# Kernel optimization log

Hardware: AMD Instinct MI355X
Metric: run time of the kernel (lower is better)

The kernel has to match this reference:

```python
import jax, jax.numpy as jnp
import numpy as np

D_MODEL, D_FF, N_EXPERTS, TOP_K = 512, 2048, 8, 2


def setup_inputs() -> dict:
    key = jax.random.key(0)
    ks = jax.random.split(key, 7)
    B, S = 2, 2048
    x = jax.random.normal(ks[0], (B, S, D_MODEL), dtype=jnp.float32)
    s1 = 1.0 / np.sqrt(D_MODEL)
    s2 = 1.0 / np.sqrt(D_FF)
    Wg = jax.random.normal(ks[1], (D_MODEL, N_EXPERTS), dtype=jnp.float32) * s1
    bg = jnp.zeros((N_EXPERTS,), dtype=jnp.float32)
    W1 = jax.random.normal(ks[2], (N_EXPERTS, D_MODEL, D_FF), dtype=jnp.float32) * s1
    b1 = jax.random.normal(ks[3], (N_EXPERTS, D_FF), dtype=jnp.float32) * s1
    W2 = jax.random.normal(ks[4], (N_EXPERTS, D_FF, D_MODEL), dtype=jnp.float32) * s2
    b2 = jax.random.normal(ks[5], (N_EXPERTS, D_MODEL), dtype=jnp.float32) * s2
    return {"x": x, "Wg": Wg, "bg": bg, "W1": W1, "b1": b1, "W2": W2, "b2": b2}


def reference(x, Wg, bg, W1, b1, W2, b2):
    B, S, D = x.shape
    xt = x.reshape(B * S, D)  # [T, D]
    # gating
    gate_logits = xt @ Wg + bg                      # [T, E]
    gate_scores = jax.nn.softmax(gate_logits, axis=-1)
    topk_scores, topk_idx = jax.lax.top_k(gate_scores, TOP_K)  # [T, K]
    topk_scores = topk_scores / jnp.sum(topk_scores, axis=-1, keepdims=True)
    # combine weights per expert: [T, E]
    combine = jnp.sum(jax.nn.one_hot(topk_idx, N_EXPERTS, dtype=xt.dtype)
                      * topk_scores[..., None], axis=1)
    # dense per-expert MLP (exact GELU, dropout is identity in eval)
    h = jax.nn.gelu(jnp.einsum('td,edf->etf', xt, W1) + b1[:, None, :],
                    approximate=False)             # [E, T, F]
    expert_out = jnp.einsum('etf,efd->etd', h, W2) + b2[:, None, :]  # [E, T, D]
    out = jnp.einsum('te,etd->td', combine, expert_out)
    return out.reshape(B, S, D)
```

## Files before the change

### kernel.cpp

```cpp
#include <hip/hip_runtime.h>
#include <hip/hip_bf16.h>
#include <math.h>

#define D_MODEL 512
#define D_FF    2048
#define NEXP    8
#define NXCD    8

using bf16x8 = __attribute__((ext_vector_type(8))) short;
using f32x4  = __attribute__((ext_vector_type(4))) float;

__device__ inline unsigned short f2bf(float x) {
    __hip_bfloat16 h = __float2bfloat16(x);
    unsigned short u; __builtin_memcpy(&u, &h, 2); return u;
}
__device__ inline unsigned pk(float a, float b) {
    return (unsigned)f2bf(a) | ((unsigned)f2bf(b) << 16);
}
__device__ inline float erf_fast(float x) {
    float ax = fabsf(x);
    float t  = 1.f / fmaf(0.3275911f, ax, 1.f);
    float p  = t * fmaf(t, fmaf(t, fmaf(t, fmaf(t, 1.061405429f, -1.453152027f),
                                        1.421413741f), -0.284496736f), 0.254829592f);
    float r  = 1.f - p * __expf(-ax * ax);
    return copysignf(r, x);
}
__device__ inline float gelu_exact(float v) {
    return 0.5f * v * (1.f + erf_fast(v * 0.70710678118654752f));
}
__device__ inline void gload_lds16(const void* g, void* l) {
    __builtin_amdgcn_global_load_lds(
        (const __attribute__((address_space(1))) unsigned int*)g,
        (__attribute__((address_space(3))) unsigned int*)l, 16, 0, 0);
}

__global__ __launch_bounds__(256) void gate_kernel(
    const float* __restrict__ x, const float* __restrict__ Wg,
    const float* __restrict__ bg,
    int2* __restrict__ tk_e, float2* __restrict__ tk_s,
    unsigned short* __restrict__ Xb, int T)
{
    int lane = threadIdx.x & 63;
    int w    = threadIdx.x >> 6;
    int t    = blockIdx.x * 4 + w;
    if (t >= T) return;

    const float* xr = x + (size_t)t * D_MODEL;
    unsigned short* xbr = Xb ? (Xb + (size_t)t * D_MODEL) : nullptr;
    float lg[NEXP];
#pragma unroll
    for (int e = 0; e < NEXP; e++) lg[e] = 0.f;

#pragma unroll
    for (int it = 0; it < D_MODEL / 64; it++) {
        int d = lane + 64 * it;
        float xv = xr[d];
        if (xbr) xbr[d] = f2bf(xv);
        const float* wr = Wg + (size_t)d * NEXP;
#pragma unroll
        for (int e = 0; e < NEXP; e++) lg[e] += xv * wr[e];
    }
#pragma unroll
    for (int off = 32; off > 0; off >>= 1) {
#pragma unroll
        for (int e = 0; e < NEXP; e++) lg[e] += __shfl_xor(lg[e], off, 64);
    }

    if (lane == 0) {
#pragma unroll
        for (int e = 0; e < NEXP; e++) lg[e] += bg[e];
        int e0 = 0;
#pragma unroll
        for (int e = 1; e < NEXP; e++) if (lg[e] > lg[e0]) e0 = e;
        int e1 = (e0 == 0) ? 1 : 0;
#pragma unroll
        for (int e = 0; e < NEXP; e++) if (e != e0 && lg[e] > lg[e1]) e1 = e;
        float s0 = 1.f / (1.f + expf(lg[e1] - lg[e0]));
        tk_e[t] = make_int2(e0, e1);
        tk_s[t] = make_float2(s0, 1.f - s0);
    }
}

__global__ __launch_bounds__(256) void route_kernel(
    const int2* __restrict__ tk_e, const float2* __restrict__ tk_s,
    int* __restrict__ counts, int* __restrict__ ltok, float* __restrict__ lsc,
    int2* __restrict__ tk_pos, int T)
{
    int t    = blockIdx.x * 256 + threadIdx.x;
    int lane = threadIdx.x & 63;
    bool valid = t < T;
    int2   es = valid ? tk_e[t] : make_int2(-1, -1);
    float2 ss = valid ? tk_s[t] : make_float2(0.f, 0.f);
    int ppos[2] = {0, 0};

#pragma unroll
    for (int slot = 0; slot < 2; slot++) {
        int   e = slot ? es.y : es.x;
        float s = slot ? ss.y : ss.x;
#pragma unroll
        for (int ex = 0; ex < NEXP; ex++) {
            unsigned long long m = __ballot(e == ex);
            if (m == 0ull) continue;
            int leader = __ffsll((long long)m) - 1;
            int base = 0;
            if (lane == leader) base = atomicAdd(&counts[ex], __popcll(m));
            base = __shfl(base, leader, 64);
            if (e == ex) {
                int pos = base + __popcll(m & ((1ull << lane) - 1ull));
                ltok[(size_t)ex * T + pos] = t;
                lsc [(size_t)ex * T + pos] = s;
                ppos[slot] = pos | (ex << 16);
            }
        }
    }
    if (valid) tk_pos[t] = make_int2(ppos[0], ppos[1]);
}

__global__ void prefix_kernel(const int* __restrict__ counts, int* __restrict__ offs)
{
    if (threadIdx.x == 0) {
        int acc = 0;
        for (int e = 0; e < NEXP; e++) { offs[e] = acc; acc += counts[e]; }
        offs[NEXP] = acc;
    }
}

__global__ __launch_bounds__(256) void tcvt2_kernel(
    const float* __restrict__ W1, const float* __restrict__ W2,
    unsigned short* __restrict__ W1t, unsigned short* __restrict__ W2t)
{
    __shared__ unsigned short tile[64][72];
    int z = blockIdx.y;
    bool isw2 = z >= NEXP;
    int e = z & (NEXP - 1);
    int R = isw2 ? D_FF : D_MODEL;
    int C = isw2 ? D_MODEL : D_FF;
    const float* src = isw2 ? W2 : W1;
    unsigned short* dst = isw2 ? W2t : W1t;

    int nx  = C / 64;
    int lin = blockIdx.x;
    int r0 = (lin / nx) * 64, c0 = (lin % nx) * 64;

    const float* s = src + ((size_t)e * R + r0) * C + c0;
    unsigned short* d = dst + ((size_t)e * C + c0) * R + r0;
    int t = threadIdx.x;
#pragma unroll
    for (int i = 0; i < 4; i++) {
        int idx = t + 256 * i;
        int r = idx >> 4, c4 = (idx & 15) * 4;
        float4 v = *(const float4*)(s + (size_t)r * C + c4);
        tile[c4    ][r] = f2bf(v.x);
        tile[c4 + 1][r] = f2bf(v.y);
        tile[c4 + 2][r] = f2bf(v.z);
        tile[c4 + 3][r] = f2bf(v.w);
    }
    __syncthreads();
#pragma unroll
    for (int i = 0; i < 2; i++) {
        int idx = t + 256 * i;
        int c = idx >> 3, q = idx & 7;
        uint4 v = *(const uint4*)(&tile[c][q * 8]);
        *(uint4*)(d + (size_t)c * R + q * 8) = v;
    }
}

__global__ __launch_bounds__(256, 4) void moe_gemm1(
    const unsigned short* __restrict__ Xb,
    const unsigned short* __restrict__ W1t, const float* __restrict__ b1,
    const int* __restrict__ counts, const int* __restrict__ offs,
    const int* __restrict__ ltok,
    unsigned short* __restrict__ Hg, int T)
{
    int nwg  = gridDim.x;
    int bid  = blockIdx.x;
    int work = (bid % NXCD) * (nwg / NXCD) + bid / NXCD;
    int perexp = nwg / NEXP;
    int e    = work / perexp;
    int rem  = work % perexp;
    int mbase = (rem >> 4) * 128;
    int fb    = (rem & 15) * 128;

    int n = counts[e];
    if (mbase >= n) return;
    int off = offs[e];

    __shared__ __align__(16) unsigned char SB[2][16384];
    __shared__ int toks_s[128];

    int tid = threadIdx.x, lane = tid & 63, w = tid >> 6;
    int wr = w & 1, wc = w >> 1;

    if (tid < 128) {
        int idx = mbase + tid; if (idx > n - 1) idx = n - 1;
        toks_s[tid] = ltok[(size_t)e * T + idx];
    }
    __syncthreads();

    const unsigned short* W1te = W1t + (size_t)e * D_FF * D_MODEL;
    int c = lane & 7, rsub = lane >> 3;

    const char* aptr[4]; const char* bptr[4]; int soff[4];
#pragma unroll
    for (int j = 0; j < 4; j++) {
        int r  = j * 32 + w * 8 + rsub;
        int sc = c ^ (r & 7);
        aptr[j] = (const char*)(Xb + (size_t)toks_s[r] * D_MODEL) + sc * 16;
        bptr[j] = (const char*)(W1te + (size_t)(fb + r) * D_MODEL) + sc * 16;
        soff[j] = (j * 32 + w * 8) * 128;
    }

    f32x4 acc[4][4];
#pragma unroll
    for (int i = 0; i < 4; i++)
#pragma unroll
        for (int j = 0; j < 4; j++) acc[i][j] = (f32x4){0.f, 0.f, 0.f, 0.f};

    for (int kc = 0; kc < D_MODEL; kc += 64) {
#pragma unroll
        for (int j = 0; j < 4; j++) gload_lds16(aptr[j] + kc * 2, SB[0] + soff[j]);
#pragma unroll
        for (int j = 0; j < 4; j++) gload_lds16(bptr[j] + kc * 2, SB[1] + soff[j]);
        __syncthreads();

#pragma unroll
        for (int ks = 0; ks < 2; ks++) {
            bf16x8 av[4], bv[4];
            int kbyte = ks * 64 + ((lane >> 4) * 16);
#pragma unroll
            for (int i = 0; i < 4; i++) {
                int row = wr * 64 + i * 16 + (lane & 15);
                av[i] = *(const bf16x8*)(SB[0] + row * 128 + (kbyte ^ ((row & 7) << 4)));
            }
#pragma unroll
            for (int j = 0; j < 4; j++) {
                int fr = wc * 64 + j * 16 + (lane & 15);
                bv[j] = *(const bf16x8*)(SB[1] + fr * 128 + (kbyte ^ ((fr & 7) << 4)));
            }
#pragma unroll
            for (int i = 0; i < 4; i++)
#pragma unroll
                for (int j = 0; j < 4; j++)
                    acc[i][j] = __builtin_amdgcn_mfma_f32_16x16x32_bf16(av[i], bv[j], acc[i][j], 0, 0, 0);
        }
        __syncthreads();
    }

    char* Eb = (char*)&SB[0][0];
    const float* b1e = b1 + (size_t)e * D_FF;
#pragma unroll
    for (int j = 0; j < 4; j++) {
        int col = wc * 64 + j * 16 + (lane & 15);
        float b1v = b1e[fb + col];
#pragma unroll
        for (int i = 0; i < 4; i++) {
#pragma unroll
            for (int r = 0; r < 4; r++) {
                int row = wr * 64 + i * 16 + (lane >> 4) * 4 + r;
                float v = gelu_exact(acc[i][j][r] + b1v);
                *(unsigned short*)(Eb + row * 256 + ((col * 2) ^ ((row & 7) << 4))) = f2bf(v);
            }
        }
    }
    __syncthreads();
#pragma unroll
    for (int k = 0; k < 8; k++) {
        int idx = tid + 256 * k;
        int row = idx >> 4, ch = idx & 15;
        if (mbase + row < n) {
            uint4 v = *(const uint4*)(Eb + row * 256 + ((ch * 16) ^ ((row & 7) << 4)));
            *(uint4*)(Hg + (size_t)(off + mbase + row) * D_FF + fb + ch * 8) = v;
        }
    }
}

__global__ __launch_bounds__(256, 4) void moe_gemm2_og(
    const unsigned short* __restrict__ Hg,
    const unsigned short* __restrict__ W2t, const float* __restrict__ b2,
    const int* __restrict__ counts, const int* __restrict__ offs,
    const int* __restrict__ ltok, const float* __restrict__ lsc,
    float* __restrict__ Og, int T)
{
    int nwg  = gridDim.x;
    int bid  = blockIdx.x;
    int work = (bid % NXCD) * (nwg / NXCD) + bid / NXCD;
    int perexp = nwg / NEXP;
    int e    = work / perexp;
    int rem  = work % perexp;
    int mbase = (rem >> 3) * 128;
    int z    = rem & 7;
    int nb   = z & 3, kb = z >> 2;
    int db   = nb * 128;

    int n = counts[e];
    if (mbase >= n) return;
    int off = offs[e];

    __shared__ __align__(16) unsigned char HsB[128 * 128];
    __shared__ __align__(16) unsigned char WsB[128 * 128];
    __shared__ float scs_s[128];

    int tid = threadIdx.x, lane = tid & 63, w = tid >> 6;
    int wr = w & 1, wc = w >> 1;

    if (tid < 128) {
        int idx = mbase + tid; if (idx > n - 1) idx = n - 1;
        scs_s[tid] = lsc[(size_t)e * T + idx];
    }
    __syncthreads();

    const unsigned short* W2te = W2t + (size_t)e * D_MODEL * D_FF;
    int c = lane & 7, rsub = lane >> 3;

    const char* aptr[4]; const char* bptr[4]; int soff[4];
#pragma unroll
    for (int j = 0; j < 4; j++) {
        int r = j * 32 + w * 8 + rsub;
        int srow = mbase + r; if (srow > n - 1) srow = n - 1;
        int sc = c ^ (r & 7);
        aptr[j] = (const char*)(Hg + (size_t)(off + srow) * D_FF) + sc * 16;
        bptr[j] = (const char*)(W2te + (size_t)(db + r) * D_FF) + sc * 16;
        soff[j] = (j * 32 + w * 8) * 128;
    }

    f32x4 acc[4][4];
#pragma unroll
    for (int i = 0; i < 4; i++)
#pragma unroll
        for (int j = 0; j < 4; j++) acc[i][j] = (f32x4){0.f, 0.f, 0.f, 0.f};

    int kbase = kb * 1024;
    for (int kc = 0; kc < 1024; kc += 64) {
        int kabs = kbase + kc;
#pragma unroll
        for (int j = 0; j < 4; j++) gload_lds16(aptr[j] + kabs * 2, HsB + soff[j]);
#pragma unroll
        for (int j = 0; j < 4; j++) gload_lds16(bptr[j] + kabs * 2, WsB + soff[j]);
        __syncthreads();

#pragma unroll
        for (int ks = 0; ks < 2; ks++) {
            bf16x8 av[4], bv[4];
            int kbyte = ks * 64 + ((lane >> 4) * 16);
#pragma unroll
            for (int i = 0; i < 4; i++) {
                int row = wr * 64 + i * 16 + (lane & 15);
                av[i] = *(const bf16x8*)(HsB + row * 128 + (kbyte ^ ((row & 7) << 4)));
            }
#pragma unroll
            for (int j = 0; j < 4; j++) {
                int dr = wc * 64 + j * 16 + (lane & 15);
                bv[j] = *(const bf16x8*)(WsB + dr * 128 + (kbyte ^ ((dr & 7) << 4)));
            }
#pragma unroll
            for (int i = 0; i < 4; i++)
#pragma unroll
                for (int j = 0; j < 4; j++)
                    acc[i][j] = __builtin_amdgcn_mfma_f32_16x16x32_bf16(av[i], bv[j], acc[i][j], 0, 0, 0);
        }
        __syncthreads();
    }

    float* Ogk = Og + (size_t)kb * (2 * T) * D_MODEL;
#pragma unroll
    for (int j = 0; j < 4; j++) {
        int dg = db + wc * 64 + j * 16 + (lane & 15);
        float b2v = (kb == 0) ? b2[(size_t)e * D_MODEL + dg] : 0.f;
#pragma unroll
        for (int i = 0; i < 4; i++) {
#pragma unroll
            for (int r = 0; r < 4; r++) {
                int rowm = wr * 64 + i * 16 + (lane >> 4) * 4 + r;
                if (mbase + rowm < n) {
                    float s = scs_s[rowm];
                    Ogk[(size_t)(off + mbase + rowm) * D_MODEL + dg] = s * (acc[i][j][r] + b2v);
                }
            }
        }
    }
}

__global__ __launch_bounds__(256) void combine_kernel(
    const float* __restrict__ Og, const int* __restrict__ offs,
    const int2* __restrict__ tk_pos, float* __restrict__ out, int T)
{
    int w = threadIdx.x >> 6, lane = threadIdx.x & 63;
    int t = blockIdx.x * 4 + w;
    if (t >= T) return;
    int2 p = tk_pos[t];
    int sA = offs[p.x >> 16] + (p.x & 0xffff);
    int sB = offs[p.y >> 16] + (p.y & 0xffff);
    size_t S = (size_t)(2 * T) * D_MODEL;
    const float4* r0 = (const float4*)(Og + (size_t)sA * D_MODEL);
    const float4* r1 = (const float4*)(Og + S + (size_t)sA * D_MODEL);
    const float4* r2 = (const float4*)(Og + (size_t)sB * D_MODEL);
    const float4* r3 = (const float4*)(Og + S + (size_t)sB * D_MODEL);
    float4* o = (float4*)(out + (size_t)t * D_MODEL);
#pragma unroll
    for (int i = 0; i < 2; i++) {
        int idx = lane + 64 * i;
        float4 a = r0[idx], b = r1[idx], cc = r2[idx], d = r3[idx];
        o[idx] = make_float4(a.x + b.x + cc.x + d.x, a.y + b.y + cc.y + d.y,
                             a.z + b.z + cc.z + d.z, a.w + b.w + cc.w + d.w);
    }
}

__global__ __launch_bounds__(256, 4) void moe_gemm2(
    const unsigned short* __restrict__ Hg,
    const unsigned short* __restrict__ W2t, const float* __restrict__ b2,
    const int* __restrict__ counts, const int* __restrict__ offs,
    const int* __restrict__ ltok, const float* __restrict__ lsc,
    float* __restrict__ out, int T)
{
    int e = blockIdx.x;
    int n = counts[e];
    int mbase = blockIdx.y * 128;
    if (mbase >= n) return;
    int nb = blockIdx.z & 3, kb = blockIdx.z >> 2;
    int db = nb * 128;
    int off = offs[e];

    __shared__ __align__(16) unsigned char HsB[128 * 128];
    __shared__ __align__(16) unsigned char WsB[128 * 128];
    __shared__ int   toks_s[128];
    __shared__ float scs_s[128];

    int tid = threadIdx.x, lane = tid & 63, w = tid >> 6;
    int wr = w & 1, wc = w >> 1;

    if (tid < 128) {
        int idx = mbase + tid; if (idx > n - 1) idx = n - 1;
        toks_s[tid] = ltok[(size_t)e * T + idx];
        scs_s [tid] = lsc [(size_t)e * T + idx];
    }
    __syncthreads();

    const unsigned short* W2te = W2t + (size_t)e * D_MODEL * D_FF;
    int c = lane & 7, rsub = lane >> 3;

    const char* aptr[4]; const char* bptr[4]; int soff[4];
#pragma unroll
    for (int j = 0; j < 4; j++) {
        int r = j * 32 + w * 8 + rsub;
        int srow = mbase + r; if (srow > n - 1) srow = n - 1;
        int sc = c ^ (r & 7);
        aptr[j] = (const char*)(Hg + (size_t)(off + srow) * D_FF) + sc * 16;
        bptr[j] = (const char*)(W2te + (size_t)(db + r) * D_FF) + sc * 16;
        soff[j] = (j * 32 + w * 8) * 128;
    }

    f32x4 acc[4][4];
#pragma unroll
    for (int i = 0; i < 4; i++)
#pragma unroll
        for (int j = 0; j < 4; j++) acc[i][j] = (f32x4){0.f, 0.f, 0.f, 0.f};

    int kbase = kb * 1024;
    for (int kc = 0; kc < 1024; kc += 64) {
        int kabs = kbase + kc;
#pragma unroll
        for (int j = 0; j < 4; j++) gload_lds16(aptr[j] + kabs * 2, HsB + soff[j]);
#pragma unroll
        for (int j = 0; j < 4; j++) gload_lds16(bptr[j] + kabs * 2, WsB + soff[j]);
        __syncthreads();

#pragma unroll
        for (int ks = 0; ks < 2; ks++) {
            bf16x8 av[4], bv[4];
            int kbyte = ks * 64 + ((lane >> 4) * 16);
#pragma unroll
            for (int i = 0; i < 4; i++) {
                int row = wr * 64 + i * 16 + (lane & 15);
                av[i] = *(const bf16x8*)(HsB + row * 128 + (kbyte ^ ((row & 7) << 4)));
            }
#pragma unroll
            for (int j = 0; j < 4; j++) {
                int dr = wc * 64 + j * 16 + (lane & 15);
                bv[j] = *(const bf16x8*)(WsB + dr * 128 + (kbyte ^ ((dr & 7) << 4)));
            }
#pragma unroll
            for (int i = 0; i < 4; i++)
#pragma unroll
                for (int j = 0; j < 4; j++)
                    acc[i][j] = __builtin_amdgcn_mfma_f32_16x16x32_bf16(av[i], bv[j], acc[i][j], 0, 0, 0);
        }
        __syncthreads();
    }

#pragma unroll
    for (int j = 0; j < 4; j++) {
        int dg = db + wc * 64 + j * 16 + (lane & 15);
        float b2v = (kb == 0) ? b2[(size_t)e * D_MODEL + dg] : 0.f;
#pragma unroll
        for (int i = 0; i < 4; i++) {
#pragma unroll
            for (int r = 0; r < 4; r++) {
                int rowm = wr * 64 + i * 16 + (lane >> 4) * 4 + r;
                if (mbase + rowm < n) {
                    float s = scs_s[rowm];
                    int tok = toks_s[rowm];
                    atomicAdd(out + (size_t)tok * D_MODEL + dg, s * (acc[i][j][r] + b2v));
                }
            }
        }
    }
}

__global__ __launch_bounds__(512, 2) void moe_gemm1_rs(
    const float* __restrict__ x,
    const float* __restrict__ W1, const float* __restrict__ b1,
    const int* __restrict__ counts, const int* __restrict__ offs,
    const int* __restrict__ ltok,
    unsigned short* __restrict__ Hg, int T)
{
    int e = blockIdx.x;
    int n = counts[e];
    int mbase = blockIdx.y * 128;
    if (mbase >= n) return;
    int fb = blockIdx.z * 256;
    int off = offs[e];

    __shared__ __align__(16) unsigned char XsB[128 * 128];
    __shared__ __align__(16) unsigned char WtB[256 * 128];
    __shared__ int toks_s[128];

    int tid  = threadIdx.x;
    int lane = tid & 63;
    int w    = tid >> 6;
    int wr   = w & 1, wc = w >> 1;

    if (tid < 128) {
        int idx = mbase + tid; if (idx > n - 1) idx = n - 1;
        toks_s[tid] = ltok[(size_t)e * T + idx];
    }
    __syncthreads();

    const float* W1e = W1 + (size_t)e * D_MODEL * D_FF;

    f32x4 acc[4][4];
#pragma unroll
    for (int i = 0; i < 4; i++)
#pragma unroll
        for (int j = 0; j < 4; j++) acc[i][j] = (f32x4){0.f, 0.f, 0.f, 0.f};

    int fcol = tid & 255, khalf = tid >> 8;
    const float* w1col = W1e + fb + fcol;

    for (int kc = 0; kc < D_MODEL; kc += 64) {
#pragma unroll
        for (int i = 0; i < 4; i++) {
            int idx = tid + 512 * i;
            int r = idx >> 4, c4 = idx & 15;
            const float4 v = *(const float4*)(x + (size_t)toks_s[r] * D_MODEL + kc + c4 * 4);
            *(uint2*)(XsB + r * 128 + ((c4 * 8) ^ ((r & 7) << 4))) =
                make_uint2(pk(v.x, v.y), pk(v.z, v.w));
        }
#pragma unroll
        for (int j = 0; j < 8; j++) {
            int q  = khalf * 8 + j;
            int k0 = kc + q * 4;
            float a0 = w1col[(size_t)(k0    ) * D_FF];
            float a1 = w1col[(size_t)(k0 + 1) * D_FF];
            float a2 = w1col[(size_t)(k0 + 2) * D_FF];
            float a3 = w1col[(size_t)(k0 + 3) * D_FF];
            *(uint2*)(WtB + fcol * 128 + ((q * 8) ^ ((fcol & 7) << 4))) =
                make_uint2(pk(a0, a1), pk(a2, a3));
        }
        __syncthreads();

#pragma unroll
        for (int ks = 0; ks < 2; ks++) {
            bf16x8 av[4], bv[4];
            int kbyte = ks * 64 + ((lane >> 4) * 16);
#pragma unroll
            for (int i = 0; i < 4; i++) {
                int row = wr * 64 + i * 16 + (lane & 15);
                av[i] = *(const bf16x8*)(XsB + row * 128 + (kbyte ^ ((row & 7) << 4)));
            }
#pragma unroll
            for (int j = 0; j < 4; j++) {
                int fr = wc * 64 + j * 16 + (lane & 15);
                bv[j] = *(const bf16x8*)(WtB + fr * 128 + (kbyte ^ ((fr & 7) << 4)));
            }
#pragma unroll
            for (int i = 0; i < 4; i++)
#pragma unroll
                for (int j = 0; j < 4; j++)
                    acc[i][j] = __builtin_amdgcn_mfma_f32_16x16x32_bf16(av[i], bv[j], acc[i][j], 0, 0, 0);
        }
        __syncthreads();
    }

    const float* b1e = b1 + (size_t)e * D_FF;
#pragma unroll
    for (int j = 0; j < 4; j++) {
        int fg = fb + wc * 64 + j * 16 + (lane & 15);
        float b1v = b1e[fg];
#pragma unroll
        for (int i = 0; i < 4; i++) {
#pragma unroll
            for (int r = 0; r < 4; r++) {
                int rowm = wr * 64 + i * 16 + (lane >> 4) * 4 + r;
                if (mbase + rowm < n) {
                    float v = gelu_exact(acc[i][j][r] + b1v);
                    Hg[(size_t)(off + mbase + rowm) * D_FF + fg] = f2bf(v);
                }
            }
        }
    }
}

__global__ __launch_bounds__(512, 2) void moe_gemm2_rs(
    const unsigned short* __restrict__ Hg,
    const float* __restrict__ W2, const float* __restrict__ b2,
    const int* __restrict__ counts, const int* __restrict__ offs,
    const int* __restrict__ ltok, const float* __restrict__ lsc,
    float* __restrict__ out, int T)
{
    int e = blockIdx.x;
    int n = counts[e];
    int mbase = blockIdx.y * 128;
    if (mbase >= n) return;
    int nb = blockIdx.z & 1, kb = blockIdx.z >> 1;
    int db = nb * 256;
    int off = offs[e];

    __shared__ __align__(16) unsigned char HsB[128 * 128];
    __shared__ __align__(16) unsigned char WtB[256 * 128];
    __shared__ int   toks_s[128];
    __shared__ float scs_s[128];

    int tid  = threadIdx.x;
    int lane = tid & 63;
    int w    = tid >> 6;
    int wr   = w & 1, wc = w >> 1;

    if (tid < 128) {
        int idx = mbase + tid; if (idx > n - 1) idx = n - 1;
        toks_s[tid] = ltok[(size_t)e * T + idx];
        scs_s [tid] = lsc [(size_t)e * T + idx];
    }
    __syncthreads();

    const float* W2e = W2 + (size_t)e * D_FF * D_MODEL;

    f32x4 acc[4][4];
#pragma unroll
    for (int i = 0; i < 4; i++)
#pragma unroll
        for (int j = 0; j < 4; j++) acc[i][j] = (f32x4){0.f, 0.f, 0.f, 0.f};

    int dcol = tid & 255, khalf = tid >> 8;
    const float* w2col = W2e + db + dcol;

    for (int kc = 0; kc < 1024; kc += 64) {
        int kabs = kb * 1024 + kc;
#pragma unroll
        for (int i = 0; i < 2; i++) {
            int idx = tid + 512 * i;
            int r = idx >> 3, c16 = idx & 7;
            int srow = mbase + r; if (srow > n - 1) srow = n - 1;
            const uint4 v = *(const uint4*)(Hg + (size_t)(off + srow) * D_FF + kabs + c16 * 8);
            *(uint4*)(HsB + r * 128 + ((c16 * 16) ^ ((r & 7) << 4))) = v;
        }
#pragma unroll
        for (int j = 0; j < 8; j++) {
            int q  = khalf * 8 + j;
            int k0 = kabs + q * 4;
            float a0 = w2col[(size_t)(k0    ) * D_MODEL];
            float a1 = w2col[(size_t)(k0 + 1) * D_MODEL];
            float a2 = w2col[(size_t)(k0 + 2) * D_MODEL];
            float a3 = w2col[(size_t)(k0 + 3) * D_MODEL];
            *(uint2*)(WtB + dcol * 128 + ((q * 8) ^ ((dcol & 7) << 4))) =
                make_uint2(pk(a0, a1), pk(a2, a3));
        }
        __syncthreads();

#pragma unroll
        for (int ks = 0; ks < 2; ks++) {
            bf16x8 av[4], bv[4];
            int kbyte = ks * 64 + ((lane >> 4) * 16);
#pragma unroll
            for (int i = 0; i < 4; i++) {
                int row = wr * 64 + i * 16 + (lane & 15);
                av[i] = *(const bf16x8*)(HsB + row * 128 + (kbyte ^ ((row & 7) << 4)));
            }
#pragma unroll
            for (int j = 0; j < 4; j++) {
                int dr = wc * 64 + j * 16 + (lane & 15);
                bv[j] = *(const bf16x8*)(WtB + dr * 128 + (kbyte ^ ((dr & 7) << 4)));
            }
#pragma unroll
            for (int i = 0; i < 4; i++)
#pragma unroll
                for (int j = 0; j < 4; j++)
                    acc[i][j] = __builtin_amdgcn_mfma_f32_16x16x32_bf16(av[i], bv[j], acc[i][j], 0, 0, 0);
        }
        __syncthreads();
    }

#pragma unroll
    for (int j = 0; j < 4; j++) {
        int dg = db + wc * 64 + j * 16 + (lane & 15);
        float b2v = (kb == 0) ? b2[(size_t)e * D_MODEL + dg] : 0.f;
#pragma unroll
        for (int i = 0; i < 4; i++) {
#pragma unroll
            for (int r = 0; r < 4; r++) {
                int rowm = wr * 64 + i * 16 + (lane >> 4) * 4 + r;
                if (mbase + rowm < n) {
                    float s = scs_s[rowm];
                    int tok = toks_s[rowm];
                    atomicAdd(out + (size_t)tok * D_MODEL + dg, s * (acc[i][j][r] + b2v));
                }
            }
        }
    }
}

extern "C" void kernel_launch(void* const* d_in, const int* in_sizes, int n_in,
                              void* d_out, int out_size, void* d_ws, size_t ws_size,
                              hipStream_t stream)
{
    const float* x  = (const float*)d_in[0];
    const float* Wg = (const float*)d_in[1];
    const float* bg = (const float*)d_in[2];
    const float* W1 = (const float*)d_in[3];
    const float* b1 = (const float*)d_in[4];
    const float* W2 = (const float*)d_in[5];
    const float* b2 = (const float*)d_in[6];
    float* out = (float*)d_out;
    int T = in_sizes[0] / D_MODEL;

    int*    counts = (int*)d_ws;
    int*    offs   = (int*)((char*)d_ws + 64);
    int*    ltok   = (int*)((char*)d_ws + 256);
    float*  lsc    = (float*)((char*)d_ws + 256 + (size_t)NEXP * T * sizeof(int));
    int2*   tk_e   = (int2*)((char*)d_ws + 256 + (size_t)2 * NEXP * T * sizeof(int));
    float2* tk_s   = (float2*)((char*)tk_e + (size_t)T * sizeof(int2));
    int2*   tk_pos = (int2*)((char*)tk_s + (size_t)T * sizeof(float2));

    const size_t Hoff   = 512 * 1024;
    const size_t Hbytes = (size_t)2 * T * D_FF * sizeof(unsigned short);
    const size_t Xoff   = Hoff + Hbytes;
    const size_t Xbytes = (size_t)T * D_MODEL * sizeof(unsigned short);
    const size_t W1off  = Xoff + Xbytes;
    const size_t Wbytes = (size_t)NEXP * D_MODEL * D_FF * sizeof(unsigned short);
    const size_t W2off  = W1off + Wbytes;
    const size_t Ogoff  = W2off + Wbytes;
    const size_t Ogbytes = (size_t)2 * (2 * T) * D_MODEL * sizeof(float);
    const size_t need_og   = Ogoff + Ogbytes + 4096;
    const size_t need_full = W2off + Wbytes + 4096;
    const size_t need_r2   = Hoff + Hbytes + 4096;

    bool og   = ws_size >= need_og;
    bool full = ws_size >= need_full;
    unsigned short* Xb = full ? (unsigned short*)((char*)d_ws + Xoff) : nullptr;

    hipMemsetAsync(d_ws, 0, 256, stream);
    if (!og)
        hipMemsetAsync(d_out, 0, (size_t)out_size * sizeof(float), stream);

    gate_kernel<<<dim3((T + 3) / 4), dim3(256), 0, stream>>>(
        x, Wg, bg, tk_e, tk_s, Xb, T);
    route_kernel<<<dim3((T + 255) / 256), dim3(256), 0, stream>>>(
        tk_e, tk_s, counts, ltok, lsc, tk_pos, T);
    prefix_kernel<<<dim3(1), dim3(64), 0, stream>>>(counts, offs);

    if (full) {
        unsigned short* Hg  = (unsigned short*)((char*)d_ws + Hoff);
        unsigned short* W1t = (unsigned short*)((char*)d_ws + W1off);
        unsigned short* W2t = (unsigned short*)((char*)d_ws + W2off);

        tcvt2_kernel<<<dim3(256, 2 * NEXP), dim3(256), 0, stream>>>(W1, W2, W1t, W2t);

        int ytiles = (T + 127) / 128;
        int g1 = NEXP * ytiles * (D_FF / 128);
        moe_gemm1<<<dim3(g1), dim3(256), 0, stream>>>(
            Xb, W1t, b1, counts, offs, ltok, Hg, T);

        if (og) {
            float* Og = (float*)((char*)d_ws + Ogoff);
            int g2 = NEXP * ytiles * 8;
            moe_gemm2_og<<<dim3(g2), dim3(256), 0, stream>>>(
                Hg, W2t, b2, counts, offs, ltok, lsc, Og, T);
            combine_kernel<<<dim3((T + 3) / 4), dim3(256), 0, stream>>>(
                Og, offs, tk_pos, out, T);
        } else {
            moe_gemm2<<<dim3(NEXP, ytiles, 8), dim3(256), 0, stream>>>(
                Hg, W2t, b2, counts, offs, ltok, lsc, out, T);
        }
    } else if (ws_size >= need_r2) {
        unsigned short* Hg = (unsigned short*)((char*)d_ws + Hoff);
        moe_gemm1_rs<<<dim3(NEXP, (T + 127) / 128, D_FF / 256), dim3(512), 0, stream>>>(
            x, W1, b1, counts, offs, ltok, Hg, T);
        moe_gemm2_rs<<<dim3(NEXP, (T + 127) / 128, 4), dim3(512), 0, stream>>>(
            Hg, W2, b2, counts, offs, ltok, lsc, out, T);
    }
}
```

Baseline: 123.9 us.

## Store GEMM2 partials in bf16 via LDS-staged writes and drop prefix kernel

The second GEMM now writes its scaled partial outputs as bf16 instead of fp32. It stages them through shared memory with a swizzled layout so each row is written as coalesced 16-byte stores. The combine kernel reads the bf16 partials and sums them in fp32. The one-thread prefix-sum kernel is removed and each kernel computes the expert offsets from counts inline, saving a launch. This halves partial-output traffic and cuts a launch, but adds bf16 rounding to the partial sums.

Result: faster. 116.4 us (-6.1%).

```diff
diff --git a/kernel.cpp b/kernel.cpp
--- a/kernel.cpp
+++ b/kernel.cpp
@@ -16,6 +16,9 @@
 }
 __device__ inline unsigned pk(float a, float b) {
     return (unsigned)f2bf(a) | ((unsigned)f2bf(b) << 16);
+}
+__device__ inline float bf2f(unsigned short u) {
+    unsigned v = (unsigned)u << 16; float f; __builtin_memcpy(&f, &v, 4); return f;
 }
 __device__ inline float erf_fast(float x) {
     float ax = fabsf(x);
@@ -32,6 +35,11 @@
     __builtin_amdgcn_global_load_lds(
         (const __attribute__((address_space(1))) unsigned int*)g,
         (__attribute__((address_space(3))) unsigned int*)l, 16, 0, 0);
+}
+__device__ inline int off_of(const int* counts, int e) {
+    int off = 0;
+    for (int i = 0; i < e; i++) off += counts[i];
+    return off;
 }
 
 __global__ __launch_bounds__(256) void gate_kernel(
@@ -116,15 +124,6 @@
     if (valid) tk_pos[t] = make_int2(ppos[0], ppos[1]);
 }
 
-__global__ void prefix_kernel(const int* __restrict__ counts, int* __restrict__ offs)
-{
-    if (threadIdx.x == 0) {
-        int acc = 0;
-        for (int e = 0; e < NEXP; e++) { offs[e] = acc; acc += counts[e]; }
-        offs[NEXP] = acc;
-    }
-}
-
 __global__ __launch_bounds__(256) void tcvt2_kernel(
     const float* __restrict__ W1, const float* __restrict__ W2,
     unsigned short* __restrict__ W1t, unsigned short* __restrict__ W2t)
@@ -168,8 +167,7 @@
 __global__ __launch_bounds__(256, 4) void moe_gemm1(
     const unsigned short* __restrict__ Xb,
     const unsigned short* __restrict__ W1t, const float* __restrict__ b1,
-    const int* __restrict__ counts, const int* __restrict__ offs,
-    const int* __restrict__ ltok,
+    const int* __restrict__ counts, const int* __restrict__ ltok,
     unsigned short* __restrict__ Hg, int T)
 {
     int nwg  = gridDim.x;
@@ -183,7 +181,7 @@
 
     int n = counts[e];
     if (mbase >= n) return;
-    int off = offs[e];
+    int off = off_of(counts, e);
 
     __shared__ __align__(16) unsigned char SB[2][16384];
     __shared__ int toks_s[128];
@@ -277,9 +275,9 @@
 __global__ __launch_bounds__(256, 4) void moe_gemm2_og(
     const unsigned short* __restrict__ Hg,
     const unsigned short* __restrict__ W2t, const float* __restrict__ b2,
-    const int* __restrict__ counts, const int* __restrict__ offs,
-    const int* __restrict__ ltok, const float* __restrict__ lsc,
-    float* __restrict__ Og, int T)
+    const int* __restrict__ counts, const int* __restrict__ ltok,
+    const float* __restrict__ lsc,
+    unsigned short* __restrict__ Og, int T)
 {
     int nwg  = gridDim.x;
     int bid  = blockIdx.x;
@@ -294,10 +292,9 @@
 
     int n = counts[e];
     if (mbase >= n) return;
-    int off = offs[e];
-
-    __shared__ __align__(16) unsigned char HsB[128 * 128];
-    __shared__ __align__(16) unsigned char WsB[128 * 128];
+    int off = off_of(counts, e);
+
+    __shared__ __align__(16) unsigned char SB[2][16384];
     __shared__ float scs_s[128];
 
     int tid = threadIdx.x, lane = tid & 63, w = tid >> 6;
@@ -333,9 +330,9 @@
     for (int kc = 0; kc < 1024; kc += 64) {
         int kabs = kbase + kc;
 #pragma unroll
-        for (int j = 0; j < 4; j++) gload_lds16(aptr[j] + kabs * 2, HsB + soff[j]);
-#pragma unroll
-        for (int j = 0; j < 4; j++) gload_lds16(bptr[j] + kabs * 2, WsB + soff[j]);
+        for (int j = 0; j < 4; j++) gload_lds16(aptr[j] + kabs * 2, SB[0] + soff[j]);
+#pragma unroll
+        for (int j = 0; j < 4; j++) gload_lds16(bptr[j] + kabs * 2, SB[1] + soff[j]);
         __syncthreads();
 
 #pragma unroll
@@ -345,12 +342,12 @@
 #pragma unroll
             for (int i = 0; i < 4; i++) {
                 int row = wr * 64 + i * 16 + (lane & 15);
-                av[i] = *(const bf16x8*)(HsB + row * 128 + (kbyte ^ ((row & 7) << 4)));
+                av[i] = *(const bf16x8*)(SB[0] + row * 128 + (kbyte ^ ((row & 7) << 4)));
             }
 #pragma unroll
             for (int j = 0; j < 4; j++) {
                 int dr = wc * 64 + j * 16 + (lane & 15);
-                bv[j] = *(const bf16x8*)(WsB + dr * 128 + (kbyte ^ ((dr & 7) << 4)));
+                bv[j] = *(const bf16x8*)(SB[1] + dr * 128 + (kbyte ^ ((dr & 7) << 4)));
             }
 #pragma unroll
             for (int i = 0; i < 4; i++)
@@ -361,55 +358,84 @@
         __syncthreads();
     }
 
-    float* Ogk = Og + (size_t)kb * (2 * T) * D_MODEL;
+    char* Eb = (char*)&SB[0][0];
 #pragma unroll
     for (int j = 0; j < 4; j++) {
-        int dg = db + wc * 64 + j * 16 + (lane & 15);
-        float b2v = (kb == 0) ? b2[(size_t)e * D_MODEL + dg] : 0.f;
+        int col = wc * 64 + j * 16 + (lane & 15);
+        float b2v = (kb == 0) ? b2[(size_t)e * D_MODEL + db + col] : 0.f;
 #pragma unroll
         for (int i = 0; i < 4; i++) {
 #pragma unroll
             for (int r = 0; r < 4; r++) {
-                int rowm = wr * 64 + i * 16 + (lane >> 4) * 4 + r;
-                if (mbase + rowm < n) {
-                    float s = scs_s[rowm];
-                    Ogk[(size_t)(off + mbase + rowm) * D_MODEL + dg] = s * (acc[i][j][r] + b2v);
-                }
-            }
+                int row = wr * 64 + i * 16 + (lane >> 4) * 4 + r;
+                float v = scs_s[row] * (acc[i][j][r] + b2v);
+                *(unsigned short*)(Eb + row * 256 + ((col * 2) ^ ((row & 7) << 4))) = f2bf(v);
+            }
+        }
+    }
+    __syncthreads();
+    unsigned short* Ogk = Og + (size_t)kb * (2 * T) * D_MODEL;
+#pragma unroll
+    for (int k = 0; k < 8; k++) {
+        int idx = tid + 256 * k;
+        int row = idx >> 4, ch = idx & 15;
+        if (mbase + row < n) {
+            uint4 v = *(const uint4*)(Eb + row * 256 + ((ch * 16) ^ ((row & 7) << 4)));
+            *(uint4*)(Ogk + (size_t)(off + mbase + row) * D_MODEL + db + ch * 8) = v;
         }
     }
 }
 
 __global__ __launch_bounds__(256) void combine_kernel(
-    const float* __restrict__ Og, const int* __restrict__ offs,
+    const unsigned short* __restrict__ Og, const int* __restrict__ counts,
     const int2* __restrict__ tk_pos, float* __restrict__ out, int T)
 {
     int w = threadIdx.x >> 6, lane = threadIdx.x & 63;
     int t = blockIdx.x * 4 + w;
     if (t >= T) return;
     int2 p = tk_pos[t];
-    int sA = offs[p.x >> 16] + (p.x & 0xffff);
-    int sB = offs[p.y >> 16] + (p.y & 0xffff);
+    int eA = p.x >> 16, eB = p.y >> 16;
+    int offA = 0, offB = 0;
+#pragma unroll
+    for (int i = 0; i < NEXP; i++) {
+        int cv = counts[i];
+        if (i < eA) offA += cv;
+        if (i < eB) offB += cv;
+    }
+    int sA = offA + (p.x & 0xffff);
+    int sB = offB + (p.y & 0xffff);
     size_t S = (size_t)(2 * T) * D_MODEL;
-    const float4* r0 = (const float4*)(Og + (size_t)sA * D_MODEL);
-    const float4* r1 = (const float4*)(Og + S + (size_t)sA * D_MODEL);
-    const float4* r2 = (const float4*)(Og + (size_t)sB * D_MODEL);
-    const float4* r3 = (const float4*)(Og + S + (size_t)sB * D_MODEL);
-    float4* o = (float4*)(out + (size_t)t * D_MODEL);
-#pragma unroll
-    for (int i = 0; i < 2; i++) {
-        int idx = lane + 64 * i;
-        float4 a = r0[idx], b = r1[idx], cc = r2[idx], d = r3[idx];
-        o[idx] = make_float4(a.x + b.x + cc.x + d.x, a.y + b.y + cc.y + d.y,
-                             a.z + b.z + cc.z + d.z, a.w + b.w + cc.w + d.w);
-    }
+    int base = lane * 8;
+    const unsigned short* r0 = Og + (size_t)sA * D_MODEL + base;
+    const unsigned short* r1 = Og + S + (size_t)sA * D_MODEL + base;
+    const unsigned short* r2 = Og + (size_t)sB * D_MODEL + base;
+    const unsigned short* r3 = Og + S + (size_t)sB * D_MODEL + base;
+
+    ushort4 a0 = *(const ushort4*)(r0), a1 = *(const ushort4*)(r0 + 4);
+    ushort4 b0 = *(const ushort4*)(r1), b1 = *(const ushort4*)(r1 + 4);
+    ushort4 c0 = *(const ushort4*)(r2), c1 = *(const ushort4*)(r2 + 4);
+    ushort4 d0 = *(const ushort4*)(r3), d1 = *(const ushort4*)(r3 + 4);
+
+    float4 o0, o1;
+    o0.x = bf2f(a0.x) + bf2f(b0.x) + bf2f(c0.x) + bf2f(d0.x);
+    o0.y = bf2f(a0.y) + bf2f(b0.y) + bf2f(c0.y) + bf2f(d0.y);
+    o0.z = bf2f(a0.z) + bf2f(b0.z) + bf2f(c0.z) + bf2f(d0.z);
+    o0.w = bf2f(a0.w) + bf2f(b0.w) + bf2f(c0.w) + bf2f(d0.w);
+    o1.x = bf2f(a1.x) + bf2f(b1.x) + bf2f(c1.x) + bf2f(d1.x);
+    o1.y = bf2f(a1.y) + bf2f(b1.y) + bf2f(c1.y) + bf2f(d1.y);
+    o1.z = bf2f(a1.z) + bf2f(b1.z) + bf2f(c1.z) + bf2f(d1.z);
+    o1.w = bf2f(a1.w) + bf2f(b1.w) + bf2f(c1.w) + bf2f(d1.w);
+
+    float* orow = out + (size_t)t * D_MODEL + base;
+    *(float4*)(orow)     = o0;
+    *(float4*)(orow + 4) = o1;
 }
 
 __global__ __launch_bounds__(256, 4) void moe_gemm2(
     const unsigned short* __restrict__ Hg,
     const unsigned short* __restrict__ W2t, const float* __restrict__ b2,
-    const int* __restrict__ counts, const int* __restrict__ offs,
-    const int* __restrict__ ltok, const float* __restrict__ lsc,
+    const int* __restrict__ counts, const int* __restrict__ ltok,
+    const float* __restrict__ lsc,
     float* __restrict__ out, int T)
 {
     int e = blockIdx.x;
@@ -418,7 +444,7 @@
     if (mbase >= n) return;
     int nb = blockIdx.z & 3, kb = blockIdx.z >> 2;
     int db = nb * 128;
-    int off = offs[e];
+    int off = off_of(counts, e);
 
     __shared__ __align__(16) unsigned char HsB[128 * 128];
     __shared__ __align__(16) unsigned char WsB[128 * 128];
@@ -509,8 +535,7 @@
 __global__ __launch_bounds__(512, 2) void moe_gemm1_rs(
     const float* __restrict__ x,
     const float* __restrict__ W1, const float* __restrict__ b1,
-    const int* __restrict__ counts, const int* __restrict__ offs,
-    const int* __restrict__ ltok,
+    const int* __restrict__ counts, const int* __restrict__ ltok,
     unsigned short* __restrict__ Hg, int T)
 {
     int e = blockIdx.x;
@@ -518,7 +543,7 @@
     int mbase = blockIdx.y * 128;
     if (mbase >= n) return;
     int fb = blockIdx.z * 256;
-    int off = offs[e];
+    int off = off_of(counts, e);
 
     __shared__ __align__(16) unsigned char XsB[128 * 128];
     __shared__ __align__(16) unsigned char WtB[256 * 128];
@@ -613,8 +638,8 @@
 __global__ __launch_bounds__(512, 2) void moe_gemm2_rs(
     const unsigned short* __restrict__ Hg,
     const float* __restrict__ W2, const float* __restrict__ b2,
-    const int* __restrict__ counts, const int* __restrict__ offs,
-    const int* __restrict__ ltok, const float* __restrict__ lsc,
+    const int* __restrict__ counts, const int* __restrict__ ltok,
+    const float* __restrict__ lsc,
     float* __restrict__ out, int T)
 {
     int e = blockIdx.x;
@@ -623,7 +648,7 @@
     if (mbase >= n) return;
     int nb = blockIdx.z & 1, kb = blockIdx.z >> 1;
     int db = nb * 256;
-    int off = offs[e];
+    int off = off_of(counts, e);
 
     __shared__ __align__(16) unsigned char HsB[128 * 128];
     __shared__ __align__(16) unsigned char WtB[256 * 128];
@@ -733,7 +758,6 @@
     int T = in_sizes[0] / D_MODEL;
 
     int*    counts = (int*)d_ws;
-    int*    offs   = (int*)((char*)d_ws + 64);
     int*    ltok   = (int*)((char*)d_ws + 256);
     float*  lsc    = (float*)((char*)d_ws + 256 + (size_t)NEXP * T * sizeof(int));
     int2*   tk_e   = (int2*)((char*)d_ws + 256 + (size_t)2 * NEXP * T * sizeof(int));
@@ -748,7 +772,7 @@
     const size_t Wbytes = (size_t)NEXP * D_MODEL * D_FF * sizeof(unsigned short);
     const size_t W2off  = W1off + Wbytes;
     const size_t Ogoff  = W2off + Wbytes;
-    const size_t Ogbytes = (size_t)2 * (2 * T) * D_MODEL * sizeof(float);
+    const size_t Ogbytes = (size_t)2 * (2 * T) * D_MODEL * sizeof(unsigned short);
     const size_t need_og   = Ogoff + Ogbytes + 4096;
     const size_t need_full = W2off + Wbytes + 4096;
     const size_t need_r2   = Hoff + Hbytes + 4096;
@@ -765,7 +789,6 @@
         x, Wg, bg, tk_e, tk_s, Xb, T);
     route_kernel<<<dim3((T + 255) / 256), dim3(256), 0, stream>>>(
         tk_e, tk_s, counts, ltok, lsc, tk_pos, T);
-    prefix_kernel<<<dim3(1), dim3(64), 0, stream>>>(counts, offs);
 
     if (full) {
         unsigned short* Hg  = (unsigned short*)((char*)d_ws + Hoff);
@@ -777,24 +800,24 @@
         int ytiles = (T + 127) / 128;
         int g1 = NEXP * ytiles * (D_FF / 128);
         moe_gemm1<<<dim3(g1), dim3(256), 0, stream>>>(
-            Xb, W1t, b1, counts, offs, ltok, Hg, T);
+            Xb, W1t, b1, counts, ltok, Hg, T);
 
         if (og) {
-            float* Og = (float*)((char*)d_ws + Ogoff);
+            unsigned short* Og = (unsigned short*)((char*)d_ws + Ogoff);
             int g2 = NEXP * ytiles * 8;
             moe_gemm2_og<<<dim3(g2), dim3(256), 0, stream>>>(
-                Hg, W2t, b2, counts, offs, ltok, lsc, Og, T);
+                Hg, W2t, b2, counts, ltok, lsc, Og, T);
             combine_kernel<<<dim3((T + 3) / 4), dim3(256), 0, stream>>>(
-                Og, offs, tk_pos, out, T);
+                Og, counts, tk_pos, out, T);
         } else {
             moe_gemm2<<<dim3(NEXP, ytiles, 8), dim3(256), 0, stream>>>(
-                Hg, W2t, b2, counts, offs, ltok, lsc, out, T);
+                Hg, W2t, b2, counts, ltok, lsc, out, T);
         }
     } else if (ws_size >= need_r2) {
         unsigned short* Hg = (unsigned short*)((char*)d_ws + Hoff);
         moe_gemm1_rs<<<dim3(NEXP, (T + 127) / 128, D_FF / 256), dim3(512), 0, stream>>>(
-            x, W1, b1, counts, offs, ltok, Hg, T);
+            x, W1, b1, counts, ltok, Hg, T);
         moe_gemm2_rs<<<dim3(NEXP, (T + 127) / 128, 4), dim3(512), 0, stream>>>(
-            Hg, W2, b2, counts, offs, ltok, lsc, out, T);
-    }
-}
+            Hg, W2, b2, counts, ltok, lsc, out, T);
+    }
+}
```
